# Kernel tuning notes

Measured on AMD Instinct MI355X. Metric: run time of the kernel, lower is better.

## Reference

```python
import jax, jax.numpy as jnp
import numpy as np

B, F, D = 1024, 256, 64  # batch, featureNumb, featureDim


def setup_inputs() -> dict:
    key = jax.random.key(0)
    k1, k2, k3, k4 = jax.random.split(key, 4)
    feature = jax.random.normal(k1, (B, F, D), dtype=jnp.float32)
    indicator = jax.random.normal(k2, (F, D), dtype=jnp.float32)
    # QKVTransformV2(n, D, D): n stacked DxD linear maps of the indicator
    W_qk = jax.random.normal(k3, (2, D, D), dtype=jnp.float32) / np.float32(np.sqrt(D))
    W_qkv = jax.random.normal(k4, (3, D, D), dtype=jnp.float32) / np.float32(np.sqrt(D))
    return {"feature": feature, "indicator": indicator, "W_qk": W_qk, "W_qkv": W_qkv}


def reference(feature, indicator, W_qk, W_qkv):
    d = indicator.shape[-1]
    scale = jnp.asarray(1.0 / np.sqrt(d), feature.dtype)

    # --- gate branch: QKTrans + DotWeight + LTE (straight-through hard threshold) ---
    trans = jnp.einsum('fd,nde->nfe', indicator, W_qk)            # [2,F,D]
    gate_logits = jnp.einsum('id,jd->ij', trans[0], trans[1]) * scale  # [F,F]
    gate = (gate_logits > 0).astype(feature.dtype)                # LTE forward: hard 0/1 gate

    # --- QKV branch, fused form of the rank-1 outer products ---
    # Original: QKV_outer[t,i,j] = qkv[t,i] (x) qkv[t,j]  (DxD rank-1)
    #           input[b,t,i,j,:] = feature[b,i] @ QKV_outer[t,i,j]
    #                            = (feature[b,i] . qkv[t,i]) * qkv[t,j]
    qkv = jnp.einsum('fd,nde->nfe', indicator, W_qkv)             # [3,F,D]
    s = jnp.einsum('bfd,nfd->nbf', feature, qkv)                  # s[t,b,i] = feature[b,i].qkv[t,i]

    # score[b,i,j] = input[b,0,i,j,:] . input[b,1,j,i,:]
    #              = s[0,b,i] * s[1,b,j] * (qkv[1,i] . qkv[0,j])
    cross = jnp.einsum('id,jd->ij', qkv[1], qkv[0])               # [F,F]
    score = s[0][:, :, None] * s[1][:, None, :] * cross[None]     # [B,F,F]
    scoreHat = score * gate[None]                                 # [B,F,F]

    # output[b,i,:] = sum_j scoreHat[b,i,j] * value[b,i,j,:]
    #               = s[2,b,i] * sum_j scoreHat[b,i,j] * qkv[2,j,:]
    out = s[2][:, :, None] * jnp.einsum('bij,jd->bid', scoreHat, qkv[2])  # [B,F,D]
    return out
```

## Files before the change

kernel.cpp:

```cpp
#include <hip/hip_runtime.h>
#include <stdint.h>

#define B 1024
#define F 256
#define D 64

typedef __attribute__((ext_vector_type(8))) short short8;
typedef __attribute__((ext_vector_type(4))) float f32x4;

__device__ __forceinline__ short f2bf(float f) {
    unsigned u = __builtin_bit_cast(unsigned, f);
    u += 0x7fff + ((u >> 16) & 1);
    return (short)(u >> 16);
}
__device__ __forceinline__ float bf2f(short s) {
    unsigned u = ((unsigned)(unsigned short)s) << 16;
    return __builtin_bit_cast(float, u);
}
__device__ __forceinline__ unsigned pk_bf16(float a, float b) {
    unsigned ua = __builtin_bit_cast(unsigned, a) + 0x8000u;
    unsigned ub = __builtin_bit_cast(unsigned, b) + 0x8000u;
    return __builtin_amdgcn_perm(ub, ua, 0x07060302u);
}


__global__ void precompute_trans(const float* __restrict__ indicator,
                                 const float* __restrict__ W_qk,
                                 const float* __restrict__ W_qkv,
                                 float* __restrict__ trans,
                                 float* __restrict__ qkv) {
    int idx = blockIdx.x * blockDim.x + threadIdx.x;
    int n   = idx / (F * D);
    int rem = idx - n * (F * D);
    int f   = rem / D;
    int e   = rem - f * D;
    const float* W = (n < 2) ? (W_qk + n * D * D) : (W_qkv + (n - 2) * D * D);
    const float* ind = indicator + f * D;
    float acc = 0.f;
#pragma unroll 8
    for (int d = 0; d < D; ++d) acc += ind[d] * W[d * D + e];
    if (n < 2) trans[n * F * D + f * D + e] = acc;
    else       qkv[(n - 2) * F * D + f * D + e] = acc;
}

__global__ __launch_bounds__(256) void compute_Mt(const float* __restrict__ trans,
                                                  const float* __restrict__ qkv,
                                                  short* __restrict__ At,
                                                  short* __restrict__ q2K) {
    int j = blockIdx.x;
    int i = threadIdx.x;
    const float4* t0 = (const float4*)(trans + i * D);
    const float4* t1 = (const float4*)(trans + F * D + j * D);
    const float4* q1 = (const float4*)(qkv + F * D + i * D);
    const float4* q0 = (const float4*)(qkv + j * D);
    float d0 = 0.f, d1 = 0.f;
#pragma unroll
    for (int k = 0; k < D / 4; ++k) {
        float4 a = t0[k], b = t1[k], c = q1[k], e = q0[k];
        d0 += a.x * b.x + a.y * b.y + a.z * b.z + a.w * b.w;
        d1 += c.x * e.x + c.y * e.y + c.z * e.z + c.w * e.w;
    }
    float v = (d0 > 0.f) ? d1 : 0.f;
    At[((j >> 5) * F + i) * 32 + (j & 31)] = f2bf(v);
    if (j < D) q2K[((i >> 5) * D + j) * 32 + (i & 31)] = f2bf(qkv[2 * F * D + i * D + j]);
}

__global__ __launch_bounds__(256) void compute_s(const float* __restrict__ feature,
                                                 const float* __restrict__ qkv,
                                                 float* __restrict__ gS,
                                                 short* __restrict__ s1S) {
    int b0 = blockIdx.x * 2;
    int rg = threadIdx.x >> 4;
    int l  = threadIdx.x & 15;
#pragma unroll 4
    for (int p = 0; p < 16; ++p) {
        int f = p * 16 + rg;
        float4 fv0 = ((const float4*)(feature + ((size_t)(b0 * F + f)) * D))[l];
        float4 fv1 = ((const float4*)(feature + ((size_t)((b0 + 1) * F + f)) * D))[l];
        float4 q0 = ((const float4*)(qkv + f * D))[l];
        float4 q1 = ((const float4*)(qkv + F * D + f * D))[l];
        float4 q2 = ((const float4*)(qkv + 2 * F * D + f * D))[l];
        float a00 = fv0.x * q0.x + fv0.y * q0.y + fv0.z * q0.z + fv0.w * q0.w;
        float a01 = fv0.x * q1.x + fv0.y * q1.y + fv0.z * q1.z + fv0.w * q1.w;
        float a02 = fv0.x * q2.x + fv0.y * q2.y + fv0.z * q2.z + fv0.w * q2.w;
        float a10 = fv1.x * q0.x + fv1.y * q0.y + fv1.z * q0.z + fv1.w * q0.w;
        float a11 = fv1.x * q1.x + fv1.y * q1.y + fv1.z * q1.z + fv1.w * q1.w;
        float a12 = fv1.x * q2.x + fv1.y * q2.y + fv1.z * q2.z + fv1.w * q2.w;
#pragma unroll
        for (int m = 1; m < 16; m <<= 1) {
            a00 += __shfl_xor(a00, m, 64);
            a01 += __shfl_xor(a01, m, 64);
            a02 += __shfl_xor(a02, m, 64);
            a10 += __shfl_xor(a10, m, 64);
            a11 += __shfl_xor(a11, m, 64);
            a12 += __shfl_xor(a12, m, 64);
        }
        if (l == 0) {
            gS[b0 * F + f]        = a00 * a02;
            gS[(b0 + 1) * F + f]  = a10 * a12;
            s1S[b0 * F + f]       = f2bf(a01);
            s1S[(b0 + 1) * F + f] = f2bf(a11);
        }
    }
}

__global__ __launch_bounds__(512, 4) void gemm_out(const short* __restrict__ At,
                                                   const short* __restrict__ q2K,
                                                   const float* __restrict__ gS,
                                                   const short* __restrict__ s1S,
                                                   float* __restrict__ out) {
    int it  = blockIdx.x & 3;
    int bg  = blockIdx.x >> 2;
    int tid = threadIdx.x;

    __shared__ __align__(16) short AtL[8 * 64 * 32];
    __shared__ __align__(16) short q2L[8 * 64 * 32];

    {
        const float4* Ag = (const float4*)At;
        const float4* Qg = (const float4*)q2K;
        float4* Al = (float4*)AtL;
        float4* Ql = (float4*)q2L;
#pragma unroll
        for (int v = tid; v < 2048; v += 512) {
            int jt = v >> 8, k = v & 255;
            Al[v] = Ag[jt * 1024 + it * 256 + k];
        }
#pragma unroll
        for (int v = tid; v < 2048; v += 512) Ql[v] = Qg[v];
    }
    __syncthreads();

    int w    = tid >> 6;
    int lane = tid & 63;
    int l16  = lane & 15;
    int lq   = lane >> 4;
    int kq   = lq * 8;
    int b    = bg * 8 + w;

    const short* s1b = s1S + b * F;

    f32x4 acc[4][4];
#pragma unroll
    for (int mt = 0; mt < 4; ++mt)
#pragma unroll
        for (int nt = 0; nt < 4; ++nt) acc[mt][nt] = (f32x4){0.f, 0.f, 0.f, 0.f};

    for (int jt = 0; jt < F / 32; ++jt) {
        short8 sv = *(const short8*)(s1b + jt * 32 + kq);
        float sf[8];
#pragma unroll
        for (int e = 0; e < 8; ++e) sf[e] = bf2f(sv[e]);

        short8 bfr[4];
#pragma unroll
        for (int nt = 0; nt < 4; ++nt) {
            int d = nt * 16 + l16;
            short8 qv = *(const short8*)(q2L + (jt * 64 + d) * 32 + kq);
            int4 packed;
            packed.x = pk_bf16(bf2f(qv[0]) * sf[0], bf2f(qv[1]) * sf[1]);
            packed.y = pk_bf16(bf2f(qv[2]) * sf[2], bf2f(qv[3]) * sf[3]);
            packed.z = pk_bf16(bf2f(qv[4]) * sf[4], bf2f(qv[5]) * sf[5]);
            packed.w = pk_bf16(bf2f(qv[6]) * sf[6], bf2f(qv[7]) * sf[7]);
            bfr[nt] = __builtin_bit_cast(short8, packed);
        }
#pragma unroll
        for (int mt = 0; mt < 4; ++mt) {
            short8 af = *(const short8*)(AtL + (jt * 64 + mt * 16 + l16) * 32 + kq);
#pragma unroll
            for (int nt = 0; nt < 4; ++nt)
                acc[mt][nt] = __builtin_amdgcn_mfma_f32_16x16x32_bf16(
                    af, bfr[nt], acc[mt][nt], 0, 0, 0);
        }
    }

    const float4* g4 = (const float4*)(gS + b * F + it * 64);
#pragma unroll
    for (int mt = 0; mt < 4; ++mt) {
        float4 gg = g4[mt * 4 + lq];
        float* obase = out + ((size_t)(b * F + it * 64 + mt * 16 + lq * 4)) * D;
#pragma unroll
        for (int nt = 0; nt < 4; ++nt) {
            float* o = obase + nt * 16 + l16;
            o[0 * D] = gg.x * acc[mt][nt][0];
            o[1 * D] = gg.y * acc[mt][nt][1];
            o[2 * D] = gg.z * acc[mt][nt][2];
            o[3 * D] = gg.w * acc[mt][nt][3];
        }
    }
}

extern "C" void kernel_launch(void* const* d_in, const int* in_sizes, int n_in,
                              void* d_out, int out_size, void* d_ws, size_t ws_size,
                              hipStream_t stream) {
    const float* feature   = (const float*)d_in[0];
    const float* indicator = (const float*)d_in[1];
    const float* W_qk      = (const float*)d_in[2];
    const float* W_qkv     = (const float*)d_in[3];
    float* out = (float*)d_out;

    float* ws    = (float*)d_ws;
    float* trans = ws;
    float* qkv   = trans + 2 * F * D;
    float* gS    = qkv + 3 * F * D;
    short* At    = (short*)(gS + B * F);
    short* q2K   = At + F * F;
    short* s1S   = q2K + (F / 32) * D * 32;

    hipLaunchKernelGGL(precompute_trans, dim3((5 * F * D) / 256), dim3(256), 0,
                       stream, indicator, W_qk, W_qkv, trans, qkv);
    hipLaunchKernelGGL(compute_Mt, dim3(F), dim3(F), 0, stream, trans, qkv, At, q2K);
    hipLaunchKernelGGL(compute_s, dim3(B / 2), dim3(256), 0, stream,
                       feature, qkv, gS, s1S);
    hipLaunchKernelGGL(gemm_out, dim3((B / 8) * 4), dim3(512), 0, stream,
                       At, q2K, gS, s1S, out);
}
```

Measured before the change: 146.2 us.

## Merge s and Mt kernels into one launch and vectorize output stores

Combines the compute_Mt and compute_s kernels into a single launch, with the block index choosing which role each block plays. This removes one launch and lets the two independent stages run concurrently. The q2K columns are permuted so that each lane's four MFMA output columns become contiguous, allowing the epilogue to write float4 stores instead of scalar strided stores. The permutation has to match the gemm's B-fragment indexing exactly, otherwise the output is silently reordered.

```diff
diff --git a/kernel.cpp b/kernel.cpp
--- a/kernel.cpp
+++ b/kernel.cpp
@@ -43,63 +43,67 @@
     else       qkv[(n - 2) * F * D + f * D + e] = acc;
 }
 
-__global__ __launch_bounds__(256) void compute_Mt(const float* __restrict__ trans,
-                                                  const float* __restrict__ qkv,
-                                                  short* __restrict__ At,
-                                                  short* __restrict__ q2K) {
-    int j = blockIdx.x;
-    int i = threadIdx.x;
-    const float4* t0 = (const float4*)(trans + i * D);
-    const float4* t1 = (const float4*)(trans + F * D + j * D);
-    const float4* q1 = (const float4*)(qkv + F * D + i * D);
-    const float4* q0 = (const float4*)(qkv + j * D);
-    float d0 = 0.f, d1 = 0.f;
-#pragma unroll
-    for (int k = 0; k < D / 4; ++k) {
-        float4 a = t0[k], b = t1[k], c = q1[k], e = q0[k];
-        d0 += a.x * b.x + a.y * b.y + a.z * b.z + a.w * b.w;
-        d1 += c.x * e.x + c.y * e.y + c.z * e.z + c.w * e.w;
-    }
-    float v = (d0 > 0.f) ? d1 : 0.f;
-    At[((j >> 5) * F + i) * 32 + (j & 31)] = f2bf(v);
-    if (j < D) q2K[((i >> 5) * D + j) * 32 + (i & 31)] = f2bf(qkv[2 * F * D + i * D + j]);
-}
-
-__global__ __launch_bounds__(256) void compute_s(const float* __restrict__ feature,
-                                                 const float* __restrict__ qkv,
-                                                 float* __restrict__ gS,
-                                                 short* __restrict__ s1S) {
-    int b0 = blockIdx.x * 2;
-    int rg = threadIdx.x >> 4;
-    int l  = threadIdx.x & 15;
+__global__ __launch_bounds__(256) void s_and_Mt(const float* __restrict__ feature,
+                                                const float* __restrict__ trans,
+                                                const float* __restrict__ qkv,
+                                                float* __restrict__ gS,
+                                                short* __restrict__ s1S,
+                                                short* __restrict__ At,
+                                                short* __restrict__ q2K) {
+    int blk = blockIdx.x;
+    if (blk < B / 2) {
+        int b0 = blk * 2;
+        int rg = threadIdx.x >> 4;
+        int l  = threadIdx.x & 15;
 #pragma unroll 4
-    for (int p = 0; p < 16; ++p) {
-        int f = p * 16 + rg;
-        float4 fv0 = ((const float4*)(feature + ((size_t)(b0 * F + f)) * D))[l];
-        float4 fv1 = ((const float4*)(feature + ((size_t)((b0 + 1) * F + f)) * D))[l];
-        float4 q0 = ((const float4*)(qkv + f * D))[l];
-        float4 q1 = ((const float4*)(qkv + F * D + f * D))[l];
-        float4 q2 = ((const float4*)(qkv + 2 * F * D + f * D))[l];
-        float a00 = fv0.x * q0.x + fv0.y * q0.y + fv0.z * q0.z + fv0.w * q0.w;
-        float a01 = fv0.x * q1.x + fv0.y * q1.y + fv0.z * q1.z + fv0.w * q1.w;
-        float a02 = fv0.x * q2.x + fv0.y * q2.y + fv0.z * q2.z + fv0.w * q2.w;
-        float a10 = fv1.x * q0.x + fv1.y * q0.y + fv1.z * q0.z + fv1.w * q0.w;
-        float a11 = fv1.x * q1.x + fv1.y * q1.y + fv1.z * q1.z + fv1.w * q1.w;
-        float a12 = fv1.x * q2.x + fv1.y * q2.y + fv1.z * q2.z + fv1.w * q2.w;
-#pragma unroll
-        for (int m = 1; m < 16; m <<= 1) {
-            a00 += __shfl_xor(a00, m, 64);
-            a01 += __shfl_xor(a01, m, 64);
-            a02 += __shfl_xor(a02, m, 64);
-            a10 += __shfl_xor(a10, m, 64);
-            a11 += __shfl_xor(a11, m, 64);
-            a12 += __shfl_xor(a12, m, 64);
-        }
-        if (l == 0) {
-            gS[b0 * F + f]        = a00 * a02;
-            gS[(b0 + 1) * F + f]  = a10 * a12;
-            s1S[b0 * F + f]       = f2bf(a01);
-            s1S[(b0 + 1) * F + f] = f2bf(a11);
+        for (int p = 0; p < 16; ++p) {
+            int f = p * 16 + rg;
+            float4 fv0 = ((const float4*)(feature + ((size_t)(b0 * F + f)) * D))[l];
+            float4 fv1 = ((const float4*)(feature + ((size_t)((b0 + 1) * F + f)) * D))[l];
+            float4 q0 = ((const float4*)(qkv + f * D))[l];
+            float4 q1 = ((const float4*)(qkv + F * D + f * D))[l];
+            float4 q2 = ((const float4*)(qkv + 2 * F * D + f * D))[l];
+            float a00 = fv0.x * q0.x + fv0.y * q0.y + fv0.z * q0.z + fv0.w * q0.w;
+            float a01 = fv0.x * q1.x + fv0.y * q1.y + fv0.z * q1.z + fv0.w * q1.w;
+            float a02 = fv0.x * q2.x + fv0.y * q2.y + fv0.z * q2.z + fv0.w * q2.w;
+            float a10 = fv1.x * q0.x + fv1.y * q0.y + fv1.z * q0.z + fv1.w * q0.w;
+            float a11 = fv1.x * q1.x + fv1.y * q1.y + fv1.z * q1.z + fv1.w * q1.w;
+            float a12 = fv1.x * q2.x + fv1.y * q2.y + fv1.z * q2.z + fv1.w * q2.w;
+#pragma unroll
+            for (int m = 1; m < 16; m <<= 1) {
+                a00 += __shfl_xor(a00, m, 64);
+                a01 += __shfl_xor(a01, m, 64);
+                a02 += __shfl_xor(a02, m, 64);
+                a10 += __shfl_xor(a10, m, 64);
+                a11 += __shfl_xor(a11, m, 64);
+                a12 += __shfl_xor(a12, m, 64);
+            }
+            if (l == 0) {
+                gS[b0 * F + f]        = a00 * a02;
+                gS[(b0 + 1) * F + f]  = a10 * a12;
+                s1S[b0 * F + f]       = f2bf(a01);
+                s1S[(b0 + 1) * F + f] = f2bf(a11);
+            }
+        }
+    } else {
+        int j = blk - B / 2;
+        int i = threadIdx.x;
+        const float4* t0 = (const float4*)(trans + i * D);
+        const float4* t1 = (const float4*)(trans + F * D + j * D);
+        const float4* q1 = (const float4*)(qkv + F * D + i * D);
+        const float4* q0 = (const float4*)(qkv + j * D);
+        float d0 = 0.f, d1 = 0.f;
+#pragma unroll
+        for (int k = 0; k < D / 4; ++k) {
+            float4 a = t0[k], b = t1[k], c = q1[k], e = q0[k];
+            d0 += a.x * b.x + a.y * b.y + a.z * b.z + a.w * b.w;
+            d1 += c.x * e.x + c.y * e.y + c.z * e.z + c.w * e.w;
+        }
+        float v = (d0 > 0.f) ? d1 : 0.f;
+        At[((j >> 5) * F + i) * 32 + (j & 31)] = f2bf(v);
+        if (j < D) {
+            int p = (j & 3) * 16 + (j >> 2);
+            q2K[((i >> 5) * D + p) * 32 + (i & 31)] = f2bf(qkv[2 * F * D + i * D + j]);
         }
     }
 }
@@ -178,15 +182,19 @@
 #pragma unroll
     for (int mt = 0; mt < 4; ++mt) {
         float4 gg = g4[mt * 4 + lq];
-        float* obase = out + ((size_t)(b * F + it * 64 + mt * 16 + lq * 4)) * D;
-#pragma unroll
-        for (int nt = 0; nt < 4; ++nt) {
-            float* o = obase + nt * 16 + l16;
-            o[0 * D] = gg.x * acc[mt][nt][0];
-            o[1 * D] = gg.y * acc[mt][nt][1];
-            o[2 * D] = gg.z * acc[mt][nt][2];
-            o[3 * D] = gg.w * acc[mt][nt][3];
-        }
+        float* obase = out + ((size_t)(b * F + it * 64 + mt * 16 + lq * 4)) * D + l16 * 4;
+        float4 v0 = {gg.x * acc[mt][0][0], gg.x * acc[mt][1][0],
+                     gg.x * acc[mt][2][0], gg.x * acc[mt][3][0]};
+        float4 v1 = {gg.y * acc[mt][0][1], gg.y * acc[mt][1][1],
+                     gg.y * acc[mt][2][1], gg.y * acc[mt][3][1]};
+        float4 v2 = {gg.z * acc[mt][0][2], gg.z * acc[mt][1][2],
+                     gg.z * acc[mt][2][2], gg.z * acc[mt][3][2]};
+        float4 v3 = {gg.w * acc[mt][0][3], gg.w * acc[mt][1][3],
+                     gg.w * acc[mt][2][3], gg.w * acc[mt][3][3]};
+        *(float4*)(obase + 0 * D) = v0;
+        *(float4*)(obase + 1 * D) = v1;
+        *(float4*)(obase + 2 * D) = v2;
+        *(float4*)(obase + 3 * D) = v3;
     }
 }
 
@@ -209,9 +217,8 @@
 
     hipLaunchKernelGGL(precompute_trans, dim3((5 * F * D) / 256), dim3(256), 0,
                        stream, indicator, W_qk, W_qkv, trans, qkv);
-    hipLaunchKernelGGL(compute_Mt, dim3(F), dim3(F), 0, stream, trans, qkv, At, q2K);
-    hipLaunchKernelGGL(compute_s, dim3(B / 2), dim3(256), 0, stream,
-                       feature, qkv, gS, s1S);
+    hipLaunchKernelGGL(s_and_Mt, dim3(B / 2 + F), dim3(256), 0, stream,
+                       feature, trans, qkv, gS, s1S, At, q2K);
     hipLaunchKernelGGL(gemm_out, dim3((B / 8) * 4), dim3(512), 0, stream,
                        At, q2K, gS, s1S, out);
 }
```

Result: faster. 142.7 us (-2.4%).
